# Performance work log

Measured on AMD Instinct MI355X. Metric: run time of the kernel, lower is better.

The kernel has to match this reference:

```python
import jax, jax.numpy as jnp
import numpy as np

N_SRC = 100000

def setup_inputs() -> dict:
    key = jax.random.key(0)
    k1, k2, k3 = jax.random.split(key, 3)
    feat_src = jax.random.normal(k1, (N_SRC, 64), dtype=jnp.float32)
    edge_src = jax.random.randint(k2, (1250000,), 0, N_SRC, dtype=jnp.int64)
    edge_dst = jax.random.randint(k3, (1250000,), 0, 50000, dtype=jnp.int64)
    return {"feat_src": feat_src, "edge_src": edge_src, "edge_dst": edge_dst, "n_dst": 50000}

def reference(feat_src, edge_src, edge_dst, n_dst):
    n_src = feat_src.shape[0]
    ones = jnp.ones(edge_src.shape[0], dtype=feat_src.dtype)
    # out-degree of src nodes, in-degree of dst nodes
    deg_out = jax.ops.segment_sum(ones, edge_src, num_segments=n_src)
    deg_in = jax.ops.segment_sum(ones, edge_dst, num_segments=n_dst)
    norm_src = jax.lax.rsqrt(jnp.clip(deg_out, 1.0))  # [n_src]
    norm_dst = jax.lax.rsqrt(jnp.clip(deg_in, 1.0))   # [n_dst]
    # gather -> scale -> scatter-sum
    msg = feat_src[edge_src] * norm_src[edge_src][:, None]      # [E, d]
    rst = jax.ops.segment_sum(msg, edge_dst, num_segments=n_dst)  # [n_dst, d]
    return rst * norm_dst[:, None]
```

## Files before the change

kernel.cpp:

```cpp
#include <hip/hip_runtime.h>

#define NFEAT 64
#define SCAN_BLOCKS 128

#define RANGE 12800
#define NB_IN 128
#define NB_OUT 64


__global__ __launch_bounds__(1024) void v25_hist(
        const int* __restrict__ idx, unsigned short* __restrict__ cnt,
        int E, int n, int Ec) {
    __shared__ int lh[RANGE];
    int b = blockIdx.x, y = blockIdx.y, t = threadIdx.x, T = blockDim.x;
    int rbase = y * RANGE;
    int rend = rbase + RANGE; if (rend > n) rend = n;
    int W = rend - rbase;
    if (W <= 0) return;
    for (int i = t; i < W; i += T) lh[i] = 0;
    __syncthreads();
    int lo = b * Ec;
    int hi = lo + Ec; if (hi > E) hi = E;
    if (lo < hi) {
        int cntE = hi - lo;
        int nq = cntE >> 2;
        for (int q = t; q < nq; q += T) {
            int i = lo + (q << 2);
            int4 e = *(const int4*)(idx + i);
            unsigned rx = (unsigned)(e.x - rbase); if (rx < (unsigned)W) atomicAdd(&lh[rx], 1);
            unsigned ry = (unsigned)(e.y - rbase); if (ry < (unsigned)W) atomicAdd(&lh[ry], 1);
            unsigned rz = (unsigned)(e.z - rbase); if (rz < (unsigned)W) atomicAdd(&lh[rz], 1);
            unsigned rw = (unsigned)(e.w - rbase); if (rw < (unsigned)W) atomicAdd(&lh[rw], 1);
        }
        for (int i = lo + (nq << 2) + t; i < hi; i += T) {
            unsigned r = (unsigned)(idx[i] - rbase);
            if (r < (unsigned)W) atomicAdd(&lh[r], 1);
        }
    }
    __syncthreads();
    unsigned short* row = cnt + (size_t)b * n + rbase;
    for (int i = t; i < W; i += T) row[i] = (unsigned short)lh[i];
}

__global__ void v25_nsrc(const unsigned short* __restrict__ cnt_out,
                         float* __restrict__ nsrc, int n_src) {
    int i = blockIdx.x * blockDim.x + threadIdx.x;
    if (i >= n_src) return;
    const unsigned short* p = cnt_out + i;
    int s = 0;
    for (int b = 0; b < NB_OUT; ++b) { s += *p; p += n_src; }
    nsrc[i] = rsqrtf(fmaxf((float)s, 1.0f));
}

__global__ void v25_prein(unsigned short* __restrict__ cnt_in,
                          int* __restrict__ deg_in, float* __restrict__ ndst,
                          int n_dst) {
    int d = blockIdx.x * blockDim.x + threadIdx.x;
    if (d >= n_dst) return;
    unsigned short* p = cnt_in + d;
    int a = 0;
    for (int b = 0; b < NB_IN; ++b) {
        int c = *p;
        *p = (unsigned short)a;
        a += c;
        p += n_dst;
    }
    deg_in[d] = a;
    ndst[d] = rsqrtf(fmaxf((float)a, 1.0f));
}

__global__ __launch_bounds__(1024) void v25_place(
        const int* __restrict__ esrc, const int* __restrict__ edst,
        const unsigned short* __restrict__ pre, const int* __restrict__ row_start,
        int* __restrict__ sorted_src, int E, int n_dst, int Ec) {
    __shared__ int lh[RANGE];
    int b = blockIdx.x, y = blockIdx.y, t = threadIdx.x, T = blockDim.x;
    int rbase = y * RANGE;
    int rend = rbase + RANGE; if (rend > n_dst) rend = n_dst;
    int W = rend - rbase;
    if (W <= 0) return;
    for (int i = t; i < W; i += T) lh[i] = 0;
    __syncthreads();
    int lo = b * Ec;
    int hi = lo + Ec; if (hi > E) hi = E;
    if (lo >= hi) return;
    const unsigned short* prow = pre + (size_t)b * n_dst;
    int cntE = hi - lo;
    int nq = cntE >> 2;
#define V25_PL(dd, ss)                                                        \
    {                                                                         \
        unsigned r = (unsigned)((dd) - rbase);                                \
        if (r < (unsigned)W) {                                                \
            int rank = atomicAdd(&lh[r], 1);                                  \
            int slot = row_start[dd] + (int)prow[dd] + rank;                  \
            if ((unsigned)slot < (unsigned)E) sorted_src[slot] = (ss);        \
        }                                                                     \
    }
    for (int q = t; q < nq; q += T) {
        int i = lo + (q << 2);
        int4 dv = *(const int4*)(edst + i);
        int4 sv = *(const int4*)(esrc + i);
        V25_PL(dv.x, sv.x)
        V25_PL(dv.y, sv.y)
        V25_PL(dv.z, sv.z)
        V25_PL(dv.w, sv.w)
    }
    for (int i = lo + (nq << 2) + t; i < hi; i += T) {
        int d = edst[i];
        int s = esrc[i];
        V25_PL(d, s)
    }
#undef V25_PL
}

__global__ void v24_gather(const float* __restrict__ feat,
                           const int* __restrict__ sorted_src,
                           const int* __restrict__ row_start,
                           const float* __restrict__ nsrc,
                           const float* __restrict__ ndst,
                           float* __restrict__ out,
                           int n_src, int n_dst) {
    int gid = blockIdx.x * blockDim.x + threadIdx.x;
    int d = gid >> 6;
    int f = threadIdx.x & 63;
    if (d >= n_dst) return;
    int lo = row_start[d], hi = row_start[d + 1];
    int nmax = n_src - 1;
    float a0 = 0, a1 = 0, a2 = 0, a3 = 0, a4 = 0, a5 = 0, a6 = 0, a7 = 0;
    int k = lo;
    for (; k + 7 < hi; k += 8) {
        int s0 = min(max(sorted_src[k    ], 0), nmax);
        int s1 = min(max(sorted_src[k + 1], 0), nmax);
        int s2 = min(max(sorted_src[k + 2], 0), nmax);
        int s3 = min(max(sorted_src[k + 3], 0), nmax);
        int s4 = min(max(sorted_src[k + 4], 0), nmax);
        int s5 = min(max(sorted_src[k + 5], 0), nmax);
        int s6 = min(max(sorted_src[k + 6], 0), nmax);
        int s7 = min(max(sorted_src[k + 7], 0), nmax);
        float v0 = feat[(size_t)s0 * NFEAT + f];
        float v1 = feat[(size_t)s1 * NFEAT + f];
        float v2 = feat[(size_t)s2 * NFEAT + f];
        float v3 = feat[(size_t)s3 * NFEAT + f];
        float v4 = feat[(size_t)s4 * NFEAT + f];
        float v5 = feat[(size_t)s5 * NFEAT + f];
        float v6 = feat[(size_t)s6 * NFEAT + f];
        float v7 = feat[(size_t)s7 * NFEAT + f];
        a0 += v0 * nsrc[s0];
        a1 += v1 * nsrc[s1];
        a2 += v2 * nsrc[s2];
        a3 += v3 * nsrc[s3];
        a4 += v4 * nsrc[s4];
        a5 += v5 * nsrc[s5];
        a6 += v6 * nsrc[s6];
        a7 += v7 * nsrc[s7];
    }
    for (; k + 3 < hi; k += 4) {
        int s0 = min(max(sorted_src[k    ], 0), nmax);
        int s1 = min(max(sorted_src[k + 1], 0), nmax);
        int s2 = min(max(sorted_src[k + 2], 0), nmax);
        int s3 = min(max(sorted_src[k + 3], 0), nmax);
        a0 += feat[(size_t)s0 * NFEAT + f] * nsrc[s0];
        a1 += feat[(size_t)s1 * NFEAT + f] * nsrc[s1];
        a2 += feat[(size_t)s2 * NFEAT + f] * nsrc[s2];
        a3 += feat[(size_t)s3 * NFEAT + f] * nsrc[s3];
    }
    for (; k < hi; ++k) {
        int s = min(max(sorted_src[k], 0), nmax);
        a0 += feat[(size_t)s * NFEAT + f] * nsrc[s];
    }
    out[d * NFEAT + f] = (((a0 + a1) + (a2 + a3)) + ((a4 + a5) + (a6 + a7))) * ndst[d];
}


__global__ void v23_scan1(const int* __restrict__ deg_in, int* __restrict__ bsum,
                          int n_dst, int chunk) {
    __shared__ int red[256];
    int b = blockIdx.x, t = threadIdx.x;
    int lo = b * chunk;
    int hi = lo + chunk; if (hi > n_dst) hi = n_dst;
    int s = 0;
    for (int i = lo + t; i < hi; i += 256) s += deg_in[i];
    red[t] = s;
    __syncthreads();
    for (int o = 128; o > 0; o >>= 1) {
        if (t < o) red[t] += red[t + o];
        __syncthreads();
    }
    if (t == 0) bsum[b] = red[0];
}

__global__ void v23_scan2(int* __restrict__ bsum, int* __restrict__ boff,
                          int* __restrict__ row_start, int n_dst) {
    if (threadIdx.x == 0) {
        int a = 0;
        for (int k = 0; k < SCAN_BLOCKS; ++k) { boff[k] = a; a += bsum[k]; }
        row_start[n_dst] = a;
    }
}

__global__ void v23_scan3(const int* __restrict__ deg_in, const int* __restrict__ boff,
                          int* __restrict__ row_start, int* __restrict__ cursor,
                          int n_dst, int chunk) {
    __shared__ int tsum[256];
    int b = blockIdx.x, t = threadIdx.x;
    int lo = b * chunk;
    int hi = lo + chunk; if (hi > n_dst) hi = n_dst;
    int per = (chunk + 255) / 256;
    int mylo = lo + t * per;
    int myhi = mylo + per; if (myhi > hi) myhi = hi;
    int s = 0;
    for (int i = mylo; i < myhi; ++i) s += deg_in[i];
    tsum[t] = s;
    __syncthreads();
    if (t == 0) {
        int a = 0;
        for (int k = 0; k < 256; ++k) { int v = tsum[k]; tsum[k] = a; a += v; }
    }
    __syncthreads();
    int a = boff[b] + tsum[t];
    for (int i = mylo; i < myhi; ++i) {
        row_start[i] = a;
        cursor[i] = a;
        a += deg_in[i];
    }
}


__global__ void v23_zero(int* __restrict__ deg_out, int* __restrict__ deg_in,
                         int n_src, int n_dst) {
    int i = blockIdx.x * blockDim.x + threadIdx.x;
    if (i < n_src) deg_out[i] = 0;
    if (i < n_dst) deg_in[i] = 0;
}

__global__ void v23_deg(const int* __restrict__ esrc, const int* __restrict__ edst,
                        int* __restrict__ deg_out, int* __restrict__ deg_in,
                        int E, int n_src, int n_dst) {
    int i = blockIdx.x * blockDim.x + threadIdx.x;
    if (i >= E) return;
    int s = esrc[i];
    int d = edst[i];
    if ((unsigned)s < (unsigned)n_src) atomicAdd(&deg_out[s], 1);
    if ((unsigned)d < (unsigned)n_dst) atomicAdd(&deg_in[d], 1);
}

__global__ void v23_norm(const int* __restrict__ deg_out, const int* __restrict__ deg_in,
                         float* __restrict__ nsrc, float* __restrict__ ndst,
                         int n_src, int n_dst) {
    int i = blockIdx.x * blockDim.x + threadIdx.x;
    if (i < n_src) nsrc[i] = rsqrtf(fmaxf((float)deg_out[i], 1.0f));
    if (i < n_dst) ndst[i] = rsqrtf(fmaxf((float)deg_in[i], 1.0f));
}

__global__ void v23_place(const int* __restrict__ esrc, const int* __restrict__ edst,
                          int* __restrict__ cursor, int* __restrict__ sorted_src,
                          int E, int n_src, int n_dst) {
    int i = blockIdx.x * blockDim.x + threadIdx.x;
    if (i >= E) return;
    int s = esrc[i];
    int d = edst[i];
    if ((unsigned)s >= (unsigned)n_src) return;
    if ((unsigned)d >= (unsigned)n_dst) return;
    int slot = atomicAdd(&cursor[d], 1);
    sorted_src[slot] = s;
}


extern "C" void kernel_launch(void* const* d_in, const int* in_sizes, int n_in,
                              void* d_out, int out_size, void* d_ws, size_t ws_size,
                              hipStream_t stream) {
    const float* feat = (const float*)d_in[0];
    const int* esrc = (const int*)d_in[1];
    const int* edst = (const int*)d_in[2];
    float* out = (float*)d_out;

    const int n_src = in_sizes[0] / NFEAT;
    const int E     = in_sizes[1];
    const int n_dst = out_size / NFEAT;

    const int B = 256;
    int nmax = n_src > n_dst ? n_src : n_dst;
    int chunk = (n_dst + SCAN_BLOCKS - 1) / SCAN_BLOCKS;

    size_t sz_cnt_in  = ((size_t)NB_IN  * (size_t)n_dst * 2 + 255) & ~(size_t)255;
    size_t sz_cnt_out = ((size_t)NB_OUT * (size_t)n_src * 2 + 255) & ~(size_t)255;
    size_t sz_fixed = (size_t)E * 4
                    + (size_t)n_dst * 4
                    + (size_t)n_src * 4
                    + (size_t)n_dst * 4
                    + (size_t)n_dst * 4
                    + (size_t)(n_dst + 1) * 4
                    + (size_t)SCAN_BLOCKS * 8 + 512;
    bool big = ws_size >= sz_cnt_in + sz_cnt_out + sz_fixed;

    if (big) {
        char* ws = (char*)d_ws;
        size_t off = 0;
        unsigned short* cnt_in  = (unsigned short*)(ws + off); off += sz_cnt_in;
        unsigned short* cnt_out = (unsigned short*)(ws + off); off += sz_cnt_out;
        int*   sorted_src = (int*)(ws + off);   off += (size_t)E * 4;
        int*   deg_in     = (int*)(ws + off);   off += (size_t)n_dst * 4;
        float* nsrc       = (float*)(ws + off); off += (size_t)n_src * 4;
        float* ndst       = (float*)(ws + off); off += (size_t)n_dst * 4;
        int*   cursor     = (int*)(ws + off);   off += (size_t)n_dst * 4;
        int*   row_start  = (int*)(ws + off);   off += (size_t)(n_dst + 1) * 4;
        int*   bsum       = (int*)(ws + off);   off += SCAN_BLOCKS * 4;
        int*   boff       = (int*)(ws + off);   off += SCAN_BLOCKS * 4;

        int Ec_in  = (((E + NB_IN  - 1) / NB_IN ) + 3) & ~3;
        int Ec_out = (((E + NB_OUT - 1) / NB_OUT) + 3) & ~3;
        int P_in  = (n_dst + RANGE - 1) / RANGE;
        int P_out = (n_src + RANGE - 1) / RANGE;

        dim3 gout(NB_OUT, P_out), gin(NB_IN, P_in);

        v25_hist<<<gout, 1024, 0, stream>>>(esrc, cnt_out, E, n_src, Ec_out);
        v25_hist<<<gin,  1024, 0, stream>>>(edst, cnt_in,  E, n_dst, Ec_in);
        v25_nsrc<<<(n_src + B - 1) / B, B, 0, stream>>>(cnt_out, nsrc, n_src);
        v25_prein<<<(n_dst + B - 1) / B, B, 0, stream>>>(cnt_in, deg_in, ndst, n_dst);
        v23_scan1<<<SCAN_BLOCKS, B, 0, stream>>>(deg_in, bsum, n_dst, chunk);
        v23_scan2<<<1, 64, 0, stream>>>(bsum, boff, row_start, n_dst);
        v23_scan3<<<SCAN_BLOCKS, B, 0, stream>>>(deg_in, boff, row_start, cursor,
                                                 n_dst, chunk);
        v25_place<<<gin, 1024, 0, stream>>>(esrc, edst, cnt_in, row_start,
                                            sorted_src, E, n_dst, Ec_in);
        long long gthreads = (long long)n_dst * 64;
        v24_gather<<<(int)((gthreads + B - 1) / B), B, 0, stream>>>(feat, sorted_src,
                                                                    row_start, nsrc, ndst,
                                                                    out, n_src, n_dst);
    } else {
        char* ws = (char*)d_ws;
        size_t off = 0;
        int*   deg_out    = (int*)(ws + off);   off += (size_t)n_src * 4;
        int*   deg_in     = (int*)(ws + off);   off += (size_t)n_dst * 4;
        float* nsrc       = (float*)(ws + off); off += (size_t)n_src * 4;
        float* ndst       = (float*)(ws + off); off += (size_t)n_dst * 4;
        int*   row_start  = (int*)(ws + off);   off += (size_t)(n_dst + 1) * 4;
        int*   cursor     = (int*)(ws + off);   off += (size_t)n_dst * 4;
        int*   bsum       = (int*)(ws + off);   off += SCAN_BLOCKS * 4;
        int*   boff       = (int*)(ws + off);   off += SCAN_BLOCKS * 4;
        int*   sorted_src = (int*)(ws + off);   off += (size_t)E * 4;

        v23_zero<<<(nmax + B - 1) / B, B, 0, stream>>>(deg_out, deg_in, n_src, n_dst);
        v23_deg<<<(E + B - 1) / B, B, 0, stream>>>(esrc, edst, deg_out, deg_in,
                                                   E, n_src, n_dst);
        v23_norm<<<(nmax + B - 1) / B, B, 0, stream>>>(deg_out, deg_in, nsrc, ndst,
                                                       n_src, n_dst);
        v23_scan1<<<SCAN_BLOCKS, B, 0, stream>>>(deg_in, bsum, n_dst, chunk);
        v23_scan2<<<1, 64, 0, stream>>>(bsum, boff, row_start, n_dst);
        v23_scan3<<<SCAN_BLOCKS, B, 0, stream>>>(deg_in, boff, row_start, cursor,
                                                 n_dst, chunk);
        v23_place<<<(E + B - 1) / B, B, 0, stream>>>(esrc, edst, cursor, sorted_src,
                                                     E, n_src, n_dst);
        long long gthreads = (long long)n_dst * 64;
        v24_gather<<<(int)((gthreads + B - 1) / B), B, 0, stream>>>(feat, sorted_src,
                                                                    row_start, nsrc, ndst,
                                                                    out, n_src, n_dst);
    }
}
```

Measured before the change: 191.9 us.

## Pack shared histograms as 16-bit pairs, fuse norm kernels, vectorize gather with float4

The histogram and placement kernels now pack two 16-bit counters into each shared int. Each block can then cover a four-times-wider node range, so far fewer grid passes over the edge list are needed, and the edge partitions per block are doubled. The nsrc and prein kernels are fused into one launch. The gather now has each 16-lane group read a full float4 row slice for a different edge and combines the groups with cross-lane shuffles. The cost is packed-counter overflow risk if more than 65535 edges in one block hit the same node, and larger intermediate count buffers.

```diff
diff --git a/kernel.cpp b/kernel.cpp
--- a/kernel.cpp
+++ b/kernel.cpp
@@ -3,83 +3,94 @@
 #define NFEAT 64
 #define SCAN_BLOCKS 128
 
-#define RANGE 12800
-#define NB_IN 128
-#define NB_OUT 64
-
-
-__global__ __launch_bounds__(1024) void v25_hist(
+#define PRANGE 51200
+#define PWORDS (PRANGE / 2)
+#define NB_IN  256
+#define NB_OUT 128
+
+__global__ __launch_bounds__(1024) void v26_hist(
         const int* __restrict__ idx, unsigned short* __restrict__ cnt,
         int E, int n, int Ec) {
-    __shared__ int lh[RANGE];
-    int b = blockIdx.x, y = blockIdx.y, t = threadIdx.x, T = blockDim.x;
-    int rbase = y * RANGE;
-    int rend = rbase + RANGE; if (rend > n) rend = n;
+    __shared__ int lh[PWORDS];
+    int b = blockIdx.x, t = threadIdx.x, T = blockDim.x;
+    int rbase = blockIdx.y * PRANGE;
+    int rend = rbase + PRANGE; if (rend > n) rend = n;
     int W = rend - rbase;
     if (W <= 0) return;
-    for (int i = t; i < W; i += T) lh[i] = 0;
+    int Wp = (W + 1) >> 1;
+    for (int i = t; i < Wp; i += T) lh[i] = 0;
     __syncthreads();
     int lo = b * Ec;
     int hi = lo + Ec; if (hi > E) hi = E;
     if (lo < hi) {
         int cntE = hi - lo;
         int nq = cntE >> 2;
+#define V26_H(val)                                                            \
+        {                                                                     \
+            unsigned r = (unsigned)((val) - rbase);                           \
+            if (r < (unsigned)W)                                              \
+                atomicAdd(&lh[r >> 1], 1 << ((r & 1) << 4));                  \
+        }
         for (int q = t; q < nq; q += T) {
             int i = lo + (q << 2);
             int4 e = *(const int4*)(idx + i);
-            unsigned rx = (unsigned)(e.x - rbase); if (rx < (unsigned)W) atomicAdd(&lh[rx], 1);
-            unsigned ry = (unsigned)(e.y - rbase); if (ry < (unsigned)W) atomicAdd(&lh[ry], 1);
-            unsigned rz = (unsigned)(e.z - rbase); if (rz < (unsigned)W) atomicAdd(&lh[rz], 1);
-            unsigned rw = (unsigned)(e.w - rbase); if (rw < (unsigned)W) atomicAdd(&lh[rw], 1);
+            V26_H(e.x) V26_H(e.y) V26_H(e.z) V26_H(e.w)
         }
-        for (int i = lo + (nq << 2) + t; i < hi; i += T) {
-            unsigned r = (unsigned)(idx[i] - rbase);
-            if (r < (unsigned)W) atomicAdd(&lh[r], 1);
+        for (int i = lo + (nq << 2) + t; i < hi; i += T) V26_H(idx[i]);
+#undef V26_H
+    }
+    __syncthreads();
+    unsigned short* row = cnt + (size_t)b * n + rbase;
+    if (((((size_t)b * n + rbase) & 1) == 0)) {
+        unsigned* row32 = (unsigned*)row;
+        int full = W >> 1;
+        for (int i = t; i < full; i += T) row32[i] = (unsigned)lh[i];
+        if ((W & 1) && t == 0)
+            row[W - 1] = (unsigned short)(lh[W >> 1] & 0xffff);
+    } else {
+        for (int i = t; i < W; i += T)
+            row[i] = (unsigned short)((lh[i >> 1] >> ((i & 1) << 4)) & 0xffff);
+    }
+}
+
+__global__ void v26_norm(const unsigned short* __restrict__ cnt_out,
+                         unsigned short* __restrict__ cnt_in,
+                         int* __restrict__ deg_in,
+                         float* __restrict__ nsrc, float* __restrict__ ndst,
+                         int n_src, int n_dst) {
+    int i = blockIdx.x * blockDim.x + threadIdx.x;
+    if (i < n_src) {
+        const unsigned short* p = cnt_out + i;
+        int s = 0;
+        for (int b = 0; b < NB_OUT; ++b) { s += *p; p += n_src; }
+        nsrc[i] = rsqrtf(fmaxf((float)s, 1.0f));
+    }
+    if (i < n_dst) {
+        unsigned short* p = cnt_in + i;
+        int a = 0;
+        for (int b = 0; b < NB_IN; ++b) {
+            int c = *p;
+            *p = (unsigned short)a;
+            a += c;
+            p += n_dst;
         }
-    }
-    __syncthreads();
-    unsigned short* row = cnt + (size_t)b * n + rbase;
-    for (int i = t; i < W; i += T) row[i] = (unsigned short)lh[i];
-}
-
-__global__ void v25_nsrc(const unsigned short* __restrict__ cnt_out,
-                         float* __restrict__ nsrc, int n_src) {
-    int i = blockIdx.x * blockDim.x + threadIdx.x;
-    if (i >= n_src) return;
-    const unsigned short* p = cnt_out + i;
-    int s = 0;
-    for (int b = 0; b < NB_OUT; ++b) { s += *p; p += n_src; }
-    nsrc[i] = rsqrtf(fmaxf((float)s, 1.0f));
-}
-
-__global__ void v25_prein(unsigned short* __restrict__ cnt_in,
-                          int* __restrict__ deg_in, float* __restrict__ ndst,
-                          int n_dst) {
-    int d = blockIdx.x * blockDim.x + threadIdx.x;
-    if (d >= n_dst) return;
-    unsigned short* p = cnt_in + d;
-    int a = 0;
-    for (int b = 0; b < NB_IN; ++b) {
-        int c = *p;
-        *p = (unsigned short)a;
-        a += c;
-        p += n_dst;
-    }
-    deg_in[d] = a;
-    ndst[d] = rsqrtf(fmaxf((float)a, 1.0f));
-}
-
-__global__ __launch_bounds__(1024) void v25_place(
+        deg_in[i] = a;
+        ndst[i] = rsqrtf(fmaxf((float)a, 1.0f));
+    }
+}
+
+__global__ __launch_bounds__(1024) void v26_place(
         const int* __restrict__ esrc, const int* __restrict__ edst,
         const unsigned short* __restrict__ pre, const int* __restrict__ row_start,
         int* __restrict__ sorted_src, int E, int n_dst, int Ec) {
-    __shared__ int lh[RANGE];
-    int b = blockIdx.x, y = blockIdx.y, t = threadIdx.x, T = blockDim.x;
-    int rbase = y * RANGE;
-    int rend = rbase + RANGE; if (rend > n_dst) rend = n_dst;
+    __shared__ int lh[PWORDS];
+    int b = blockIdx.x, t = threadIdx.x, T = blockDim.x;
+    int rbase = blockIdx.y * PRANGE;
+    int rend = rbase + PRANGE; if (rend > n_dst) rend = n_dst;
     int W = rend - rbase;
     if (W <= 0) return;
-    for (int i = t; i < W; i += T) lh[i] = 0;
+    int Wp = (W + 1) >> 1;
+    for (int i = t; i < Wp; i += T) lh[i] = 0;
     __syncthreads();
     int lo = b * Ec;
     int hi = lo + Ec; if (hi > E) hi = E;
@@ -87,11 +98,13 @@
     const unsigned short* prow = pre + (size_t)b * n_dst;
     int cntE = hi - lo;
     int nq = cntE >> 2;
-#define V25_PL(dd, ss)                                                        \
+#define V26_PL(dd, ss)                                                        \
     {                                                                         \
         unsigned r = (unsigned)((dd) - rbase);                                \
         if (r < (unsigned)W) {                                                \
-            int rank = atomicAdd(&lh[r], 1);                                  \
+            int sh = (r & 1) << 4;                                            \
+            int old = atomicAdd(&lh[r >> 1], 1 << sh);                        \
+            int rank = (old >> sh) & 0xffff;                                  \
             int slot = row_start[dd] + (int)prow[dd] + rank;                  \
             if ((unsigned)slot < (unsigned)E) sorted_src[slot] = (ss);        \
         }                                                                     \
@@ -100,20 +113,20 @@
         int i = lo + (q << 2);
         int4 dv = *(const int4*)(edst + i);
         int4 sv = *(const int4*)(esrc + i);
-        V25_PL(dv.x, sv.x)
-        V25_PL(dv.y, sv.y)
-        V25_PL(dv.z, sv.z)
-        V25_PL(dv.w, sv.w)
+        V26_PL(dv.x, sv.x)
+        V26_PL(dv.y, sv.y)
+        V26_PL(dv.z, sv.z)
+        V26_PL(dv.w, sv.w)
     }
     for (int i = lo + (nq << 2) + t; i < hi; i += T) {
         int d = edst[i];
         int s = esrc[i];
-        V25_PL(d, s)
-    }
-#undef V25_PL
-}
-
-__global__ void v24_gather(const float* __restrict__ feat,
+        V26_PL(d, s)
+    }
+#undef V26_PL
+}
+
+__global__ void v26_gather(const float* __restrict__ feat,
                            const int* __restrict__ sorted_src,
                            const int* __restrict__ row_start,
                            const float* __restrict__ nsrc,
@@ -122,53 +135,51 @@
                            int n_src, int n_dst) {
     int gid = blockIdx.x * blockDim.x + threadIdx.x;
     int d = gid >> 6;
-    int f = threadIdx.x & 63;
     if (d >= n_dst) return;
+    int lane = threadIdx.x & 63;
+    int g = lane >> 4;
+    int lg = lane & 15;
     int lo = row_start[d], hi = row_start[d + 1];
     int nmax = n_src - 1;
-    float a0 = 0, a1 = 0, a2 = 0, a3 = 0, a4 = 0, a5 = 0, a6 = 0, a7 = 0;
+    float4 a0 = {0,0,0,0}, a1 = {0,0,0,0}, a2 = {0,0,0,0}, a3 = {0,0,0,0};
+#define V26_G(kk, acc)                                                        \
+    {                                                                         \
+        int s_ = sorted_src[(kk) + g];                                        \
+        s_ = min(max(s_, 0), nmax);                                           \
+        float w_ = nsrc[s_];                                                  \
+        float4 v_ = *(const float4*)(feat + (size_t)s_ * NFEAT + (lg << 2));  \
+        acc.x += v_.x * w_; acc.y += v_.y * w_;                               \
+        acc.z += v_.z * w_; acc.w += v_.w * w_;                               \
+    }
     int k = lo;
-    for (; k + 7 < hi; k += 8) {
-        int s0 = min(max(sorted_src[k    ], 0), nmax);
-        int s1 = min(max(sorted_src[k + 1], 0), nmax);
-        int s2 = min(max(sorted_src[k + 2], 0), nmax);
-        int s3 = min(max(sorted_src[k + 3], 0), nmax);
-        int s4 = min(max(sorted_src[k + 4], 0), nmax);
-        int s5 = min(max(sorted_src[k + 5], 0), nmax);
-        int s6 = min(max(sorted_src[k + 6], 0), nmax);
-        int s7 = min(max(sorted_src[k + 7], 0), nmax);
-        float v0 = feat[(size_t)s0 * NFEAT + f];
-        float v1 = feat[(size_t)s1 * NFEAT + f];
-        float v2 = feat[(size_t)s2 * NFEAT + f];
-        float v3 = feat[(size_t)s3 * NFEAT + f];
-        float v4 = feat[(size_t)s4 * NFEAT + f];
-        float v5 = feat[(size_t)s5 * NFEAT + f];
-        float v6 = feat[(size_t)s6 * NFEAT + f];
-        float v7 = feat[(size_t)s7 * NFEAT + f];
-        a0 += v0 * nsrc[s0];
-        a1 += v1 * nsrc[s1];
-        a2 += v2 * nsrc[s2];
-        a3 += v3 * nsrc[s3];
-        a4 += v4 * nsrc[s4];
-        a5 += v5 * nsrc[s5];
-        a6 += v6 * nsrc[s6];
-        a7 += v7 * nsrc[s7];
+    for (; k + 15 < hi; k += 16) {
+        V26_G(k, a0)
+        V26_G(k + 4, a1)
+        V26_G(k + 8, a2)
+        V26_G(k + 12, a3)
     }
     for (; k + 3 < hi; k += 4) {
-        int s0 = min(max(sorted_src[k    ], 0), nmax);
-        int s1 = min(max(sorted_src[k + 1], 0), nmax);
-        int s2 = min(max(sorted_src[k + 2], 0), nmax);
-        int s3 = min(max(sorted_src[k + 3], 0), nmax);
-        a0 += feat[(size_t)s0 * NFEAT + f] * nsrc[s0];
-        a1 += feat[(size_t)s1 * NFEAT + f] * nsrc[s1];
-        a2 += feat[(size_t)s2 * NFEAT + f] * nsrc[s2];
-        a3 += feat[(size_t)s3 * NFEAT + f] * nsrc[s3];
-    }
-    for (; k < hi; ++k) {
-        int s = min(max(sorted_src[k], 0), nmax);
-        a0 += feat[(size_t)s * NFEAT + f] * nsrc[s];
-    }
-    out[d * NFEAT + f] = (((a0 + a1) + (a2 + a3)) + ((a4 + a5) + (a6 + a7))) * ndst[d];
+        V26_G(k, a0)
+    }
+    if (k + g < hi) {
+        V26_G(k, a1)
+    }
+#undef V26_G
+    float4 a;
+    a.x = (a0.x + a1.x) + (a2.x + a3.x);
+    a.y = (a0.y + a1.y) + (a2.y + a3.y);
+    a.z = (a0.z + a1.z) + (a2.z + a3.z);
+    a.w = (a0.w + a1.w) + (a2.w + a3.w);
+    a.x += __shfl_xor(a.x, 16); a.x += __shfl_xor(a.x, 32);
+    a.y += __shfl_xor(a.y, 16); a.y += __shfl_xor(a.y, 32);
+    a.z += __shfl_xor(a.z, 16); a.z += __shfl_xor(a.z, 32);
+    a.w += __shfl_xor(a.w, 16); a.w += __shfl_xor(a.w, 32);
+    if (g == 0) {
+        float sc = ndst[d];
+        float4 r;
+        r.x = a.x * sc; r.y = a.y * sc; r.z = a.z * sc; r.w = a.w * sc;
+        *(float4*)(out + (size_t)d * NFEAT + (lg << 2)) = r;
+    }
 }
 
 
@@ -309,23 +320,23 @@
 
         int Ec_in  = (((E + NB_IN  - 1) / NB_IN ) + 3) & ~3;
         int Ec_out = (((E + NB_OUT - 1) / NB_OUT) + 3) & ~3;
-        int P_in  = (n_dst + RANGE - 1) / RANGE;
-        int P_out = (n_src + RANGE - 1) / RANGE;
+        int P_in  = (n_dst + PRANGE - 1) / PRANGE;
+        int P_out = (n_src + PRANGE - 1) / PRANGE;
 
         dim3 gout(NB_OUT, P_out), gin(NB_IN, P_in);
 
-        v25_hist<<<gout, 1024, 0, stream>>>(esrc, cnt_out, E, n_src, Ec_out);
-        v25_hist<<<gin,  1024, 0, stream>>>(edst, cnt_in,  E, n_dst, Ec_in);
-        v25_nsrc<<<(n_src + B - 1) / B, B, 0, stream>>>(cnt_out, nsrc, n_src);
-        v25_prein<<<(n_dst + B - 1) / B, B, 0, stream>>>(cnt_in, deg_in, ndst, n_dst);
+        v26_hist<<<gout, 1024, 0, stream>>>(esrc, cnt_out, E, n_src, Ec_out);
+        v26_hist<<<gin,  1024, 0, stream>>>(edst, cnt_in,  E, n_dst, Ec_in);
+        v26_norm<<<(nmax + B - 1) / B, B, 0, stream>>>(cnt_out, cnt_in, deg_in,
+                                                       nsrc, ndst, n_src, n_dst);
         v23_scan1<<<SCAN_BLOCKS, B, 0, stream>>>(deg_in, bsum, n_dst, chunk);
         v23_scan2<<<1, 64, 0, stream>>>(bsum, boff, row_start, n_dst);
         v23_scan3<<<SCAN_BLOCKS, B, 0, stream>>>(deg_in, boff, row_start, cursor,
                                                  n_dst, chunk);
-        v25_place<<<gin, 1024, 0, stream>>>(esrc, edst, cnt_in, row_start,
+        v26_place<<<gin, 1024, 0, stream>>>(esrc, edst, cnt_in, row_start,
                                             sorted_src, E, n_dst, Ec_in);
         long long gthreads = (long long)n_dst * 64;
-        v24_gather<<<(int)((gthreads + B - 1) / B), B, 0, stream>>>(feat, sorted_src,
+        v26_gather<<<(int)((gthreads + B - 1) / B), B, 0, stream>>>(feat, sorted_src,
                                                                     row_start, nsrc, ndst,
                                                                     out, n_src, n_dst);
     } else {
@@ -353,7 +364,7 @@
         v23_place<<<(E + B - 1) / B, B, 0, stream>>>(esrc, edst, cursor, sorted_src,
                                                      E, n_src, n_dst);
         long long gthreads = (long long)n_dst * 64;
-        v24_gather<<<(int)((gthreads + B - 1) / B), B, 0, stream>>>(feat, sorted_src,
+        v26_gather<<<(int)((gthreads + B - 1) / B), B, 0, stream>>>(feat, sorted_src,
                                                                     row_start, nsrc, ndst,
                                                                     out, n_src, n_dst);
     }
```

Result: slower. 214.5 us (+11.8%).
